# Optimization experiments

Hardware: AMD Instinct MI355X
Metric: run time of the kernel (lower is better)

## Reference

```python
import jax, jax.numpy as jnp
import numpy as np

B, T = 64, 2000
Q_DIM, MEM_DIM, ATT_DIM = 1024, 512, 128
N_FILTERS, KERNEL = 32, 31


def setup_inputs() -> dict:
    key = jax.random.key(0)
    ks = jax.random.split(key, 8)
    s = lambda fan_in: 1.0 / np.sqrt(fan_in)
    return {
        "attention_hidden_state": jax.random.normal(ks[0], (B, Q_DIM), jnp.float32),
        "memory": jax.random.normal(ks[1], (B, T, MEM_DIM), jnp.float32),
        "attention_weights_cat": jax.random.uniform(ks[2], (B, 2, T), jnp.float32),
        "W_query": jax.random.normal(ks[3], (Q_DIM, ATT_DIM), jnp.float32) * s(Q_DIM),
        "W_memory": jax.random.normal(ks[4], (MEM_DIM, ATT_DIM), jnp.float32) * s(MEM_DIM),
        "W_v": jax.random.normal(ks[5], (ATT_DIM, 1), jnp.float32) * s(ATT_DIM),
        "W_conv": jax.random.normal(ks[6], (KERNEL, 2, N_FILTERS), jnp.float32) * s(KERNEL * 2),  # WIO layout
        "W_loc": jax.random.normal(ks[7], (N_FILTERS, ATT_DIM), jnp.float32) * s(N_FILTERS),
    }


def reference(attention_hidden_state, memory, attention_weights_cat,
              W_query, W_memory, W_v, W_conv, W_loc):
    # processed query: [B, 1, D]
    pq = jnp.tanh(attention_hidden_state @ W_query)[:, None, :]
    # processed memory: [B, T, D]
    pm = jnp.tanh(jnp.einsum('btm,md->btd', memory, W_memory))
    # location features: Conv1D 'same', no bias, channels-last input [B, T, 2]
    awc = jnp.transpose(attention_weights_cat, (0, 2, 1))
    conv = jax.lax.conv_general_dilated(
        awc, W_conv, window_strides=(1,), padding='SAME',
        dimension_numbers=('NWC', 'WIO', 'NWC'))  # [B, T, F]
    ploc = jnp.tanh(conv @ W_loc)  # [B, T, D]
    # energies: [B, T]
    energies = jnp.squeeze(jnp.tanh(pq + ploc + pm) @ W_v, -1)
    attention_weights = jax.nn.softmax(energies, axis=1)  # [B, T]
    attention_context = jnp.einsum('bt,btm->bm', attention_weights, memory)
    return attention_context, attention_weights
```

## Files before the change

### kernel.cpp

```cpp
#include <hip/hip_runtime.h>
#include <hip/hip_bf16.h>

typedef __attribute__((ext_vector_type(8))) short s16x8;
typedef __attribute__((ext_vector_type(4))) float f32x4;

#define B_SZ 64
#define T_SZ 2000
#define QD 1024
#define MD 512
#define AD 128
#define NF 32
#define KW 31
#define NTILE 63
#define ASTRIDE 1056

__device__ __forceinline__ unsigned short f2bf(float f) {
    unsigned int u = __float_as_uint(f);
    unsigned int r = (u + 0x7FFFu + ((u >> 16) & 1u)) >> 16;
    return (unsigned short)r;
}
__device__ __forceinline__ unsigned int pack2bf_manual(float a, float b) {
    return (unsigned int)f2bf(a) | ((unsigned int)f2bf(b) << 16);
}
__device__ __forceinline__ unsigned int pack2bf(float a, float b) {
    union { __hip_bfloat162 h; unsigned int u; } cv;
    cv.h = __float22bfloat162_rn(float2{a, b});
    return cv.u;
}
__device__ __forceinline__ float fast_tanh(float x) {
    float ax = fabsf(x);
    float e = __expf(2.0f * ax);
    float r = 1.0f - 2.0f * __builtin_amdgcn_rcpf(e + 1.0f);
    return x < 0.0f ? -r : r;
}

__global__ __launch_bounds__(512) void prep_kernel(
    const float* __restrict__ ahs, const float* __restrict__ Wq,
    const float* __restrict__ Wm, const float* __restrict__ Wl,
    float* __restrict__ pq, unsigned short* __restrict__ WB,
    unsigned short* __restrict__ WL) {
    const int blk = blockIdx.x, tid = threadIdx.x;
    if (blk < 64) {
        __shared__ float q_sm[QD];
        __shared__ float part[3][AD];
        ((float2*)q_sm)[tid] = ((const float2*)(ahs + blk * QD))[tid];
        __syncthreads();
        const int d = tid & 127, kh = tid >> 7;
        const int k0 = kh * 256;
        float a0 = 0, a1 = 0, a2 = 0, a3 = 0;
        #pragma unroll 4
        for (int k = k0; k < k0 + 256; k += 4) {
            a0 += q_sm[k]     * Wq[(k)     * AD + d];
            a1 += q_sm[k + 1] * Wq[(k + 1) * AD + d];
            a2 += q_sm[k + 2] * Wq[(k + 2) * AD + d];
            a3 += q_sm[k + 3] * Wq[(k + 3) * AD + d];
        }
        float s = (a0 + a1) + (a2 + a3);
        if (kh) part[kh - 1][d] = s;
        __syncthreads();
        if (tid < AD)
            pq[blk * AD + tid] =
                fast_tanh((s + part[0][tid]) + (part[1][tid] + part[2][tid]));
    } else if (blk < 80) {
        int cidx = (blk - 64) * 512 + tid;
        int n = cidx >> 10, s = (cidx >> 6) & 15, l = cidx & 63;
        int col = n * 16 + (l & 15);
        int krow = s * 32 + (l >> 4) * 8;
        float v[8];
        #pragma unroll
        for (int j = 0; j < 8; ++j) v[j] = Wm[(krow + j) * AD + col];
        uint4 pk;
        pk.x = pack2bf(v[0], v[1]); pk.y = pack2bf(v[2], v[3]);
        pk.z = pack2bf(v[4], v[5]); pk.w = pack2bf(v[6], v[7]);
        *(uint4*)(WB + cidx * 8) = pk;
    } else {
        int cidx = tid;
        int n = cidx >> 6, l = cidx & 63;
        int col = n * 16 + (l & 15);
        int krow = (l >> 4) * 8;
        float v[8];
        #pragma unroll
        for (int j = 0; j < 8; ++j) v[j] = Wl[(krow + j) * AD + col];
        uint4 pk;
        pk.x = pack2bf_manual(v[0], v[1]); pk.y = pack2bf_manual(v[2], v[3]);
        pk.z = pack2bf_manual(v[4], v[5]); pk.w = pack2bf_manual(v[6], v[7]);
        *(uint4*)(WL + cidx * 8) = pk;
    }
}

__global__ __launch_bounds__(256) void energy_kernel(
    const float* __restrict__ memory, const float* __restrict__ awcat,
    const float* __restrict__ Wconv, const float* __restrict__ Wv,
    const float* __restrict__ pq, const unsigned short* __restrict__ WB,
    const unsigned short* __restrict__ WL, float* __restrict__ wts,
    float* __restrict__ ctile, float* __restrict__ mloc,
    float* __restrict__ Stile) {
    const int tile = blockIdx.x;
    const int b = blockIdx.y;
    const int t0 = tile * 32;
    const int tid = threadIdx.x;

    __shared__ __align__(16) unsigned short Atile[32 * (ASTRIDE / 2)];
    __shared__ float aw_sm[2][64];
    __shared__ __align__(16) unsigned short conv_sm[32 * 40];
    __shared__ float e_part[32][4];
    __shared__ float p_sm[32];

    if (tid < 128) {
        int c = tid >> 6, i = tid & 63;
        float v = 0.0f;
        int tv = t0 - 15 + i;
        if (i < 63 && tv >= 0 && tv < T_SZ) v = awcat[(b * 2 + c) * T_SZ + tv];
        aw_sm[c][i] = v;
    }

    {
        const float4* msrc = (const float4*)(memory + ((size_t)b * T_SZ + t0) * MD);
        #pragma unroll
        for (int it = 0; it < 8; ++it) {
            int cid = it * 256 + tid;
            int r = cid >> 6, cc = cid & 63;
            float4 v0 = {0, 0, 0, 0}, v1 = {0, 0, 0, 0};
            if (t0 + r < T_SZ) {
                v0 = msrc[r * 128 + cc * 2];
                v1 = msrc[r * 128 + cc * 2 + 1];
            }
            uint4 pk;
            pk.x = pack2bf(v0.x, v0.y); pk.y = pack2bf(v0.z, v0.w);
            pk.z = pack2bf(v1.x, v1.y); pk.w = pack2bf(v1.z, v1.w);
            int off = r * ASTRIDE + ((cc * 16) ^ ((r & 7) << 4));
            *(uint4*)((char*)Atile + off) = pk;
        }
    }
    __syncthreads();

    {
        int f = tid & 31, tq = tid >> 5;
        float acc[4] = {0, 0, 0, 0};
        for (int k = 0; k < KW; ++k) {
            #pragma unroll
            for (int c = 0; c < 2; ++c) {
                float wv = Wconv[(k * 2 + c) * NF + f];
                #pragma unroll
                for (int tt = 0; tt < 4; ++tt)
                    acc[tt] += wv * aw_sm[c][tq + tt * 8 + k];
            }
        }
        #pragma unroll
        for (int tt = 0; tt < 4; ++tt)
            conv_sm[(tq + tt * 8) * 40 + f] = f2bf(acc[tt]);
    }
    __syncthreads();

    const int w = tid >> 6, l = tid & 63;
    const int lr = l & 15, lg = l >> 4;
    const int d0 = (2 * w + 0) * 16 + lr;
    const int d1 = (2 * w + 1) * 16 + lr;
    const float pqv0 = pq[b * AD + d0], pqv1 = pq[b * AD + d1];
    const float wvv0 = Wv[d0], wvv1 = Wv[d1];

    f32x4 zero4 = {0, 0, 0, 0};
    f32x4 p00 = zero4, p01 = zero4, p10 = zero4, p11 = zero4;

    const s16x8* wbp = (const s16x8*)WB;
    const int swz = (lr & 7) << 4;
    const int rbase0 = lr * ASTRIDE;
    const int rbase1 = (16 + lr) * ASTRIDE;
    const int inb = lg * 16;

    #pragma unroll
    for (int s = 0; s < 16; ++s) {
        int j = (inb + s * 64) ^ swz;
        s16x8 a0 = *(const s16x8*)((const char*)Atile + rbase0 + j);
        s16x8 a1 = *(const s16x8*)((const char*)Atile + rbase1 + j);
        s16x8 b0 = wbp[((2 * w + 0) * 16 + s) * 64 + l];
        s16x8 b1 = wbp[((2 * w + 1) * 16 + s) * 64 + l];
        p00 = __builtin_amdgcn_mfma_f32_16x16x32_bf16(a0, b0, p00, 0, 0, 0);
        p01 = __builtin_amdgcn_mfma_f32_16x16x32_bf16(a0, b1, p01, 0, 0, 0);
        p10 = __builtin_amdgcn_mfma_f32_16x16x32_bf16(a1, b0, p10, 0, 0, 0);
        p11 = __builtin_amdgcn_mfma_f32_16x16x32_bf16(a1, b1, p11, 0, 0, 0);
    }

    s16x8 la0 = *(const s16x8*)((const char*)conv_sm + (lr * 80 + lg * 16));
    s16x8 la1 = *(const s16x8*)((const char*)conv_sm + ((16 + lr) * 80 + lg * 16));
    const s16x8* wlp = (const s16x8*)WL;
    s16x8 lb0 = wlp[(2 * w + 0) * 64 + l];
    s16x8 lb1 = wlp[(2 * w + 1) * 64 + l];
    f32x4 q00 = __builtin_amdgcn_mfma_f32_16x16x32_bf16(la0, lb0, zero4, 0, 0, 0);
    f32x4 q01 = __builtin_amdgcn_mfma_f32_16x16x32_bf16(la0, lb1, zero4, 0, 0, 0);
    f32x4 q10 = __builtin_amdgcn_mfma_f32_16x16x32_bf16(la1, lb0, zero4, 0, 0, 0);
    f32x4 q11 = __builtin_amdgcn_mfma_f32_16x16x32_bf16(la1, lb1, zero4, 0, 0, 0);

    float vr[8];
    #pragma unroll
    for (int r = 0; r < 4; ++r) {
        vr[r]     = fast_tanh(pqv0 + fast_tanh(q00[r]) + fast_tanh(p00[r])) * wvv0
                  + fast_tanh(pqv1 + fast_tanh(q01[r]) + fast_tanh(p01[r])) * wvv1;
        vr[4 + r] = fast_tanh(pqv0 + fast_tanh(q10[r]) + fast_tanh(p10[r])) * wvv0
                  + fast_tanh(pqv1 + fast_tanh(q11[r]) + fast_tanh(p11[r])) * wvv1;
    }
    #pragma unroll
    for (int j = 0; j < 8; ++j) {
        float v = vr[j];
        v += __shfl_xor(v, 1);
        v += __shfl_xor(v, 2);
        v += __shfl_xor(v, 4);
        v += __shfl_xor(v, 8);
        if (lr == 0) e_part[(j >> 2) * 16 + lg * 4 + (j & 3)][w] = v;
    }
    __syncthreads();

    if (tid < 32) {
        int t = t0 + tid;
        bool valid = t < T_SZ;
        float e = (e_part[tid][0] + e_part[tid][1]) + (e_part[tid][2] + e_part[tid][3]);
        float m = valid ? e : -3.4e38f;
        m = fmaxf(m, __shfl_xor(m, 1));
        m = fmaxf(m, __shfl_xor(m, 2));
        m = fmaxf(m, __shfl_xor(m, 4));
        m = fmaxf(m, __shfl_xor(m, 8));
        m = fmaxf(m, __shfl_xor(m, 16));
        float p = valid ? __expf(e - m) : 0.0f;
        p_sm[tid] = p;
        float S = p;
        S += __shfl_xor(S, 1);
        S += __shfl_xor(S, 2);
        S += __shfl_xor(S, 4);
        S += __shfl_xor(S, 8);
        S += __shfl_xor(S, 16);
        if (valid) wts[b * T_SZ + t] = p;
        if (tid == 0) { mloc[b * NTILE + tile] = m; Stile[b * NTILE + tile] = S; }
    }
    __syncthreads();

    {
        float c0 = 0.0f, c1 = 0.0f;
        const int boff = tid * 4;
        #pragma unroll
        for (int t = 0; t < 32; ++t) {
            float p = p_sm[t];
            unsigned int pk = *(const unsigned int*)(
                (const char*)Atile + t * ASTRIDE + (boff ^ ((t & 7) << 4)));
            c0 += p * __uint_as_float(pk << 16);
            c1 += p * __uint_as_float(pk & 0xffff0000u);
        }
        float2 o; o.x = c0; o.y = c1;
        ((float2*)ctile)[((b * NTILE + tile) << 8) + tid] = o;
    }
}

__global__ __launch_bounds__(256) void finalize_kernel(
    const float* __restrict__ mloc, const float* __restrict__ Stile,
    const float* __restrict__ ctile, float* __restrict__ wts,
    float* __restrict__ ctx) {
    const int b = blockIdx.x, h = blockIdx.y, tid = threadIdx.x;
    __shared__ float sc_sm[NTILE + 1];
    if (tid < 64) {
        float m = (tid < NTILE) ? mloc[b * NTILE + tid] : -3.4e38f;
        float s = (tid < NTILE) ? Stile[b * NTILE + tid] : 0.0f;
        float M = m;
        M = fmaxf(M, __shfl_xor(M, 1));  M = fmaxf(M, __shfl_xor(M, 2));
        M = fmaxf(M, __shfl_xor(M, 4));  M = fmaxf(M, __shfl_xor(M, 8));
        M = fmaxf(M, __shfl_xor(M, 16)); M = fmaxf(M, __shfl_xor(M, 32));
        float e = __expf(m - M);
        float z = e * s;
        z += __shfl_xor(z, 1);  z += __shfl_xor(z, 2);
        z += __shfl_xor(z, 4);  z += __shfl_xor(z, 8);
        z += __shfl_xor(z, 16); z += __shfl_xor(z, 32);
        if (tid < NTILE) sc_sm[tid] = e / z;
    }
    __syncthreads();

    if (h == 0) {
        #pragma unroll
        for (int i = 0; i < 8; ++i) {
            int idx = tid + i * 256;
            if (idx < T_SZ) wts[b * T_SZ + idx] *= sc_sm[idx >> 5];
        }
    }

    float a = 0.0f;
    const float* cb = ctile + ((size_t)b * NTILE << 9) + h * 256 + tid;
    #pragma unroll 7
    for (int tl = 0; tl < NTILE; ++tl) a += sc_sm[tl] * cb[(size_t)tl << 9];
    ctx[b * MD + h * 256 + tid] = a;
}

extern "C" void kernel_launch(void* const* d_in, const int* in_sizes, int n_in,
                              void* d_out, int out_size, void* d_ws, size_t ws_size,
                              hipStream_t stream) {
    const float* ahs    = (const float*)d_in[0];
    const float* memory = (const float*)d_in[1];
    const float* awcat  = (const float*)d_in[2];
    const float* Wq     = (const float*)d_in[3];
    const float* Wm     = (const float*)d_in[4];
    const float* Wv     = (const float*)d_in[5];
    const float* Wconv  = (const float*)d_in[6];
    const float* Wl     = (const float*)d_in[7];

    float* out = (float*)d_out;
    float* ctx = out;
    float* wts = out + B_SZ * MD;

    char* ws = (char*)d_ws;
    float* pq             = (float*)(ws);
    unsigned short* WB    = (unsigned short*)(ws + 32768);
    unsigned short* WL    = (unsigned short*)(ws + 163840);
    float* mloc           = (float*)(ws + 172032);
    float* Stile          = (float*)(ws + 188160);
    float* ctile          = (float*)(ws + 204800);

    prep_kernel<<<81, 512, 0, stream>>>(ahs, Wq, Wm, Wl, pq, WB, WL);
    energy_kernel<<<dim3(NTILE, B_SZ), 256, 0, stream>>>(
        memory, awcat, Wconv, Wv, pq, WB, WL, wts, ctile, mloc, Stile);
    finalize_kernel<<<dim3(B_SZ, 2), 256, 0, stream>>>(mloc, Stile, ctile, wts, ctx);
}
```

Baseline: 91.40 us.

## Halve energy tile to 16 timesteps and add unfused context fallback path

```diff
diff --git a/kernel.cpp b/kernel.cpp
--- a/kernel.cpp
+++ b/kernel.cpp
@@ -11,7 +11,8 @@
 #define AD 128
 #define NF 32
 #define KW 31
-#define NTILE 63
+#define TT 16
+#define NTILE 125
 #define ASTRIDE 1056
 
 __device__ __forceinline__ unsigned short f2bf(float f) {
@@ -88,43 +89,32 @@
     }
 }
 
-__global__ __launch_bounds__(256) void energy_kernel(
+__global__ __launch_bounds__(256, 6) void energy_kernel(
     const float* __restrict__ memory, const float* __restrict__ awcat,
     const float* __restrict__ Wconv, const float* __restrict__ Wv,
     const float* __restrict__ pq, const unsigned short* __restrict__ WB,
     const unsigned short* __restrict__ WL, float* __restrict__ wts,
     float* __restrict__ ctile, float* __restrict__ mloc,
-    float* __restrict__ Stile) {
+    float* __restrict__ Stile, int do_fuse) {
     const int tile = blockIdx.x;
     const int b = blockIdx.y;
-    const int t0 = tile * 32;
+    const int t0 = tile * TT;
     const int tid = threadIdx.x;
 
-    __shared__ __align__(16) unsigned short Atile[32 * (ASTRIDE / 2)];
+    __shared__ __align__(16) unsigned short Atile[TT * (ASTRIDE / 2)];
     __shared__ float aw_sm[2][64];
-    __shared__ __align__(16) unsigned short conv_sm[32 * 40];
-    __shared__ float e_part[32][4];
-    __shared__ float p_sm[32];
-
-    if (tid < 128) {
-        int c = tid >> 6, i = tid & 63;
-        float v = 0.0f;
-        int tv = t0 - 15 + i;
-        if (i < 63 && tv >= 0 && tv < T_SZ) v = awcat[(b * 2 + c) * T_SZ + tv];
-        aw_sm[c][i] = v;
-    }
+    __shared__ __align__(16) unsigned short conv_sm[TT * 40];
+    __shared__ float e_part[TT][4];
+    __shared__ float p_sm[TT];
 
     {
         const float4* msrc = (const float4*)(memory + ((size_t)b * T_SZ + t0) * MD);
         #pragma unroll
-        for (int it = 0; it < 8; ++it) {
+        for (int it = 0; it < 4; ++it) {
             int cid = it * 256 + tid;
             int r = cid >> 6, cc = cid & 63;
-            float4 v0 = {0, 0, 0, 0}, v1 = {0, 0, 0, 0};
-            if (t0 + r < T_SZ) {
-                v0 = msrc[r * 128 + cc * 2];
-                v1 = msrc[r * 128 + cc * 2 + 1];
-            }
+            float4 v0 = msrc[r * 128 + cc * 2];
+            float4 v1 = msrc[r * 128 + cc * 2 + 1];
             uint4 pk;
             pk.x = pack2bf(v0.x, v0.y); pk.y = pack2bf(v0.z, v0.w);
             pk.z = pack2bf(v1.x, v1.y); pk.w = pack2bf(v1.z, v1.w);
@@ -132,23 +122,29 @@
             *(uint4*)((char*)Atile + off) = pk;
         }
     }
+
+    if (tid < 128) {
+        int c = tid >> 6, i = tid & 63;
+        float v = 0.0f;
+        int tv = t0 - 15 + i;
+        if (i < 46 && tv >= 0 && tv < T_SZ) v = awcat[(b * 2 + c) * T_SZ + tv];
+        aw_sm[c][i] = v;
+    }
     __syncthreads();
 
     {
         int f = tid & 31, tq = tid >> 5;
-        float acc[4] = {0, 0, 0, 0};
+        float acc[2] = {0, 0};
         for (int k = 0; k < KW; ++k) {
             #pragma unroll
             for (int c = 0; c < 2; ++c) {
                 float wv = Wconv[(k * 2 + c) * NF + f];
-                #pragma unroll
-                for (int tt = 0; tt < 4; ++tt)
-                    acc[tt] += wv * aw_sm[c][tq + tt * 8 + k];
+                acc[0] += wv * aw_sm[c][tq + k];
+                acc[1] += wv * aw_sm[c][tq + 8 + k];
             }
         }
-        #pragma unroll
-        for (int tt = 0; tt < 4; ++tt)
-            conv_sm[(tq + tt * 8) * 40 + f] = f2bf(acc[tt]);
+        conv_sm[(tq)     * 40 + f] = f2bf(acc[0]);
+        conv_sm[(tq + 8) * 40 + f] = f2bf(acc[1]);
     }
     __syncthreads();
 
@@ -160,87 +156,70 @@
     const float wvv0 = Wv[d0], wvv1 = Wv[d1];
 
     f32x4 zero4 = {0, 0, 0, 0};
-    f32x4 p00 = zero4, p01 = zero4, p10 = zero4, p11 = zero4;
+    f32x4 p00 = zero4, p01 = zero4;
 
     const s16x8* wbp = (const s16x8*)WB;
     const int swz = (lr & 7) << 4;
-    const int rbase0 = lr * ASTRIDE;
-    const int rbase1 = (16 + lr) * ASTRIDE;
+    const int rbase = lr * ASTRIDE;
     const int inb = lg * 16;
+    const char* Ac = (const char*)Atile;
 
     #pragma unroll
     for (int s = 0; s < 16; ++s) {
         int j = (inb + s * 64) ^ swz;
-        s16x8 a0 = *(const s16x8*)((const char*)Atile + rbase0 + j);
-        s16x8 a1 = *(const s16x8*)((const char*)Atile + rbase1 + j);
+        s16x8 a0 = *(const s16x8*)(Ac + rbase + j);
         s16x8 b0 = wbp[((2 * w + 0) * 16 + s) * 64 + l];
         s16x8 b1 = wbp[((2 * w + 1) * 16 + s) * 64 + l];
         p00 = __builtin_amdgcn_mfma_f32_16x16x32_bf16(a0, b0, p00, 0, 0, 0);
         p01 = __builtin_amdgcn_mfma_f32_16x16x32_bf16(a0, b1, p01, 0, 0, 0);
-        p10 = __builtin_amdgcn_mfma_f32_16x16x32_bf16(a1, b0, p10, 0, 0, 0);
-        p11 = __builtin_amdgcn_mfma_f32_16x16x32_bf16(a1, b1, p11, 0, 0, 0);
     }
 
     s16x8 la0 = *(const s16x8*)((const char*)conv_sm + (lr * 80 + lg * 16));
-    s16x8 la1 = *(const s16x8*)((const char*)conv_sm + ((16 + lr) * 80 + lg * 16));
     const s16x8* wlp = (const s16x8*)WL;
     s16x8 lb0 = wlp[(2 * w + 0) * 64 + l];
     s16x8 lb1 = wlp[(2 * w + 1) * 64 + l];
     f32x4 q00 = __builtin_amdgcn_mfma_f32_16x16x32_bf16(la0, lb0, zero4, 0, 0, 0);
     f32x4 q01 = __builtin_amdgcn_mfma_f32_16x16x32_bf16(la0, lb1, zero4, 0, 0, 0);
-    f32x4 q10 = __builtin_amdgcn_mfma_f32_16x16x32_bf16(la1, lb0, zero4, 0, 0, 0);
-    f32x4 q11 = __builtin_amdgcn_mfma_f32_16x16x32_bf16(la1, lb1, zero4, 0, 0, 0);
-
-    float vr[8];
+
     #pragma unroll
     for (int r = 0; r < 4; ++r) {
-        vr[r]     = fast_tanh(pqv0 + fast_tanh(q00[r]) + fast_tanh(p00[r])) * wvv0
-                  + fast_tanh(pqv1 + fast_tanh(q01[r]) + fast_tanh(p01[r])) * wvv1;
-        vr[4 + r] = fast_tanh(pqv0 + fast_tanh(q10[r]) + fast_tanh(p10[r])) * wvv0
-                  + fast_tanh(pqv1 + fast_tanh(q11[r]) + fast_tanh(p11[r])) * wvv1;
-    }
-    #pragma unroll
-    for (int j = 0; j < 8; ++j) {
-        float v = vr[j];
+        float v = fast_tanh(pqv0 + fast_tanh(q00[r]) + fast_tanh(p00[r])) * wvv0
+                + fast_tanh(pqv1 + fast_tanh(q01[r]) + fast_tanh(p01[r])) * wvv1;
         v += __shfl_xor(v, 1);
         v += __shfl_xor(v, 2);
         v += __shfl_xor(v, 4);
         v += __shfl_xor(v, 8);
-        if (lr == 0) e_part[(j >> 2) * 16 + lg * 4 + (j & 3)][w] = v;
-    }
-    __syncthreads();
-
-    if (tid < 32) {
-        int t = t0 + tid;
-        bool valid = t < T_SZ;
+        if (lr == 0) e_part[lg * 4 + r][w] = v;
+    }
+    __syncthreads();
+
+    if (tid < TT) {
         float e = (e_part[tid][0] + e_part[tid][1]) + (e_part[tid][2] + e_part[tid][3]);
-        float m = valid ? e : -3.4e38f;
+        float m = e;
         m = fmaxf(m, __shfl_xor(m, 1));
         m = fmaxf(m, __shfl_xor(m, 2));
         m = fmaxf(m, __shfl_xor(m, 4));
         m = fmaxf(m, __shfl_xor(m, 8));
-        m = fmaxf(m, __shfl_xor(m, 16));
-        float p = valid ? __expf(e - m) : 0.0f;
+        float p = __expf(e - m);
         p_sm[tid] = p;
         float S = p;
         S += __shfl_xor(S, 1);
         S += __shfl_xor(S, 2);
         S += __shfl_xor(S, 4);
         S += __shfl_xor(S, 8);
-        S += __shfl_xor(S, 16);
-        if (valid) wts[b * T_SZ + t] = p;
+        wts[b * T_SZ + t0 + tid] = p;
         if (tid == 0) { mloc[b * NTILE + tile] = m; Stile[b * NTILE + tile] = S; }
     }
     __syncthreads();
 
-    {
+    if (do_fuse) {
         float c0 = 0.0f, c1 = 0.0f;
         const int boff = tid * 4;
         #pragma unroll
-        for (int t = 0; t < 32; ++t) {
+        for (int t = 0; t < TT; ++t) {
             float p = p_sm[t];
             unsigned int pk = *(const unsigned int*)(
-                (const char*)Atile + t * ASTRIDE + (boff ^ ((t & 7) << 4)));
+                Ac + t * ASTRIDE + (boff ^ ((t & 7) << 4)));
             c0 += p * __uint_as_float(pk << 16);
             c1 += p * __uint_as_float(pk & 0xffff0000u);
         }
@@ -252,22 +231,27 @@
 __global__ __launch_bounds__(256) void finalize_kernel(
     const float* __restrict__ mloc, const float* __restrict__ Stile,
     const float* __restrict__ ctile, float* __restrict__ wts,
-    float* __restrict__ ctx) {
+    float* __restrict__ ctx, int do_fuse) {
     const int b = blockIdx.x, h = blockIdx.y, tid = threadIdx.x;
-    __shared__ float sc_sm[NTILE + 1];
+    __shared__ float sc_sm[128];
     if (tid < 64) {
-        float m = (tid < NTILE) ? mloc[b * NTILE + tid] : -3.4e38f;
-        float s = (tid < NTILE) ? Stile[b * NTILE + tid] : 0.0f;
-        float M = m;
+        float ma = mloc[b * NTILE + tid];
+        float sa = Stile[b * NTILE + tid];
+        bool hasb = (tid + 64) < NTILE;
+        float mb = hasb ? mloc[b * NTILE + tid + 64] : -3.4e38f;
+        float sb = hasb ? Stile[b * NTILE + tid + 64] : 0.0f;
+        float M = fmaxf(ma, mb);
         M = fmaxf(M, __shfl_xor(M, 1));  M = fmaxf(M, __shfl_xor(M, 2));
         M = fmaxf(M, __shfl_xor(M, 4));  M = fmaxf(M, __shfl_xor(M, 8));
         M = fmaxf(M, __shfl_xor(M, 16)); M = fmaxf(M, __shfl_xor(M, 32));
-        float e = __expf(m - M);
-        float z = e * s;
+        float ea = __expf(ma - M), eb = hasb ? __expf(mb - M) : 0.0f;
+        float z = ea * sa + eb * sb;
         z += __shfl_xor(z, 1);  z += __shfl_xor(z, 2);
         z += __shfl_xor(z, 4);  z += __shfl_xor(z, 8);
         z += __shfl_xor(z, 16); z += __shfl_xor(z, 32);
-        if (tid < NTILE) sc_sm[tid] = e / z;
+        float inv = 1.0f / z;
+        sc_sm[tid] = ea * inv;
+        sc_sm[tid + 64] = eb * inv;
     }
     __syncthreads();
 
@@ -275,15 +259,47 @@
         #pragma unroll
         for (int i = 0; i < 8; ++i) {
             int idx = tid + i * 256;
-            if (idx < T_SZ) wts[b * T_SZ + idx] *= sc_sm[idx >> 5];
-        }
-    }
-
-    float a = 0.0f;
-    const float* cb = ctile + ((size_t)b * NTILE << 9) + h * 256 + tid;
-    #pragma unroll 7
-    for (int tl = 0; tl < NTILE; ++tl) a += sc_sm[tl] * cb[(size_t)tl << 9];
-    ctx[b * MD + h * 256 + tid] = a;
+            if (idx < T_SZ) wts[b * T_SZ + idx] *= sc_sm[idx >> 4];
+        }
+    }
+
+    if (do_fuse) {
+        float a = 0.0f;
+        const float* cb = ctile + ((size_t)b * NTILE << 9) + h * 256 + tid;
+        #pragma unroll 5
+        for (int tl = 0; tl < NTILE; ++tl) a += sc_sm[tl] * cb[(size_t)tl << 9];
+        ctx[b * MD + h * 256 + tid] = a;
+    }
+}
+
+__global__ __launch_bounds__(256) void ctx_partial_kernel(
+    const float* __restrict__ memory, const float* __restrict__ wts,
+    float* __restrict__ part) {
+    const int ci = blockIdx.x, b = blockIdx.y, tid = threadIdx.x;
+    const float2* m2 = (const float2*)memory;
+    float2 acc = {0.0f, 0.0f};
+    const int t0 = ci * 100, t1 = t0 + 100;
+    #pragma unroll 4
+    for (int t = t0; t < t1; ++t) {
+        float wgt = wts[b * T_SZ + t];
+        float2 v = m2[((size_t)(b * T_SZ + t)) * 256 + tid];
+        acc.x += wgt * v.x;
+        acc.y += wgt * v.y;
+    }
+    ((float2*)part)[(b * 20 + ci) * 256 + tid] = acc;
+}
+__global__ __launch_bounds__(256) void ctx_reduce_kernel(
+    const float* __restrict__ part, float* __restrict__ ctx) {
+    const int b = blockIdx.x, tid = threadIdx.x;
+    const float2* p2 = (const float2*)part;
+    float2 acc = {0.0f, 0.0f};
+    #pragma unroll
+    for (int ci = 0; ci < 20; ++ci) {
+        float2 v = p2[(b * 20 + ci) * 256 + tid];
+        acc.x += v.x;
+        acc.y += v.y;
+    }
+    ((float2*)ctx)[b * 256 + tid] = acc;
 }
 
 extern "C" void kernel_launch(void* const* d_in, const int* in_sizes, int n_in,
@@ -307,11 +323,20 @@
     unsigned short* WB    = (unsigned short*)(ws + 32768);
     unsigned short* WL    = (unsigned short*)(ws + 163840);
     float* mloc           = (float*)(ws + 172032);
-    float* Stile          = (float*)(ws + 188160);
-    float* ctile          = (float*)(ws + 204800);
+    float* Stile          = (float*)(ws + 204800);
+    float* ctile          = (float*)(ws + 237568);
+    float* part           = (float*)(ws + 237568);
+
+    const size_t need_fused = 237568 + (size_t)B_SZ * NTILE * MD * 4;
+    const int do_fuse = (ws_size >= need_fused) ? 1 : 0;
 
     prep_kernel<<<81, 512, 0, stream>>>(ahs, Wq, Wm, Wl, pq, WB, WL);
     energy_kernel<<<dim3(NTILE, B_SZ), 256, 0, stream>>>(
-        memory, awcat, Wconv, Wv, pq, WB, WL, wts, ctile, mloc, Stile);
-    finalize_kernel<<<dim3(B_SZ, 2), 256, 0, stream>>>(mloc, Stile, ctile, wts, ctx);
-}
+        memory, awcat, Wconv, Wv, pq, WB, WL, wts, ctile, mloc, Stile, do_fuse);
+    finalize_kernel<<<dim3(B_SZ, 2), 256, 0, stream>>>(
+        mloc, Stile, ctile, wts, ctx, do_fuse);
+    if (!do_fuse) {
+        ctx_partial_kernel<<<dim3(20, B_SZ), 256, 0, stream>>>(memory, wts, part);
+        ctx_reduce_kernel<<<B_SZ, 256, 0, stream>>>(part, ctx);
+    }
+}
```

New measurement: 103.4 us. 1.13x slower.

## Feed MFMA operands directly from global memory instead of staging in LDS

Applied to the files above, without the earlier changes.

```diff
diff --git a/kernel.cpp b/kernel.cpp
--- a/kernel.cpp
+++ b/kernel.cpp
@@ -12,7 +12,6 @@
 #define NF 32
 #define KW 31
 #define NTILE 63
-#define ASTRIDE 1056
 
 __device__ __forceinline__ unsigned short f2bf(float f) {
     unsigned int u = __float_as_uint(f);
@@ -26,6 +25,12 @@
     union { __hip_bfloat162 h; unsigned int u; } cv;
     cv.h = __float22bfloat162_rn(float2{a, b});
     return cv.u;
+}
+__device__ __forceinline__ s16x8 pack8(float4 x0, float4 x1) {
+    union { s16x8 v; uint4 u; } r;
+    r.u.x = pack2bf(x0.x, x0.y); r.u.y = pack2bf(x0.z, x0.w);
+    r.u.z = pack2bf(x1.x, x1.y); r.u.w = pack2bf(x1.z, x1.w);
+    return r.v;
 }
 __device__ __forceinline__ float fast_tanh(float x) {
     float ax = fabsf(x);
@@ -88,7 +93,7 @@
     }
 }
 
-__global__ __launch_bounds__(256) void energy_kernel(
+__global__ __launch_bounds__(256, 4) void energy_kernel(
     const float* __restrict__ memory, const float* __restrict__ awcat,
     const float* __restrict__ Wconv, const float* __restrict__ Wv,
     const float* __restrict__ pq, const unsigned short* __restrict__ WB,
@@ -99,8 +104,8 @@
     const int b = blockIdx.y;
     const int t0 = tile * 32;
     const int tid = threadIdx.x;
-
-    __shared__ __align__(16) unsigned short Atile[32 * (ASTRIDE / 2)];
+    const bool full = (t0 + 32 <= T_SZ);
+
     __shared__ float aw_sm[2][64];
     __shared__ __align__(16) unsigned short conv_sm[32 * 40];
     __shared__ float e_part[32][4];
@@ -112,25 +117,6 @@
         int tv = t0 - 15 + i;
         if (i < 63 && tv >= 0 && tv < T_SZ) v = awcat[(b * 2 + c) * T_SZ + tv];
         aw_sm[c][i] = v;
-    }
-
-    {
-        const float4* msrc = (const float4*)(memory + ((size_t)b * T_SZ + t0) * MD);
-        #pragma unroll
-        for (int it = 0; it < 8; ++it) {
-            int cid = it * 256 + tid;
-            int r = cid >> 6, cc = cid & 63;
-            float4 v0 = {0, 0, 0, 0}, v1 = {0, 0, 0, 0};
-            if (t0 + r < T_SZ) {
-                v0 = msrc[r * 128 + cc * 2];
-                v1 = msrc[r * 128 + cc * 2 + 1];
-            }
-            uint4 pk;
-            pk.x = pack2bf(v0.x, v0.y); pk.y = pack2bf(v0.z, v0.w);
-            pk.z = pack2bf(v1.x, v1.y); pk.w = pack2bf(v1.z, v1.w);
-            int off = r * ASTRIDE + ((cc * 16) ^ ((r & 7) << 4));
-            *(uint4*)((char*)Atile + off) = pk;
-        }
     }
     __syncthreads();
 
@@ -163,22 +149,33 @@
     f32x4 p00 = zero4, p01 = zero4, p10 = zero4, p11 = zero4;
 
     const s16x8* wbp = (const s16x8*)WB;
-    const int swz = (lr & 7) << 4;
-    const int rbase0 = lr * ASTRIDE;
-    const int rbase1 = (16 + lr) * ASTRIDE;
-    const int inb = lg * 16;
-
-    #pragma unroll
-    for (int s = 0; s < 16; ++s) {
-        int j = (inb + s * 64) ^ swz;
-        s16x8 a0 = *(const s16x8*)((const char*)Atile + rbase0 + j);
-        s16x8 a1 = *(const s16x8*)((const char*)Atile + rbase1 + j);
-        s16x8 b0 = wbp[((2 * w + 0) * 16 + s) * 64 + l];
-        s16x8 b1 = wbp[((2 * w + 1) * 16 + s) * 64 + l];
-        p00 = __builtin_amdgcn_mfma_f32_16x16x32_bf16(a0, b0, p00, 0, 0, 0);
-        p01 = __builtin_amdgcn_mfma_f32_16x16x32_bf16(a0, b1, p01, 0, 0, 0);
-        p10 = __builtin_amdgcn_mfma_f32_16x16x32_bf16(a1, b0, p10, 0, 0, 0);
-        p11 = __builtin_amdgcn_mfma_f32_16x16x32_bf16(a1, b1, p11, 0, 0, 0);
+    const float4* m0 = (const float4*)(memory + ((size_t)b * T_SZ + t0 + lr) * MD) + lg * 2;
+
+    if (full) {
+        const float4* m1 = m0 + 16 * (MD / 4);
+        #pragma unroll 4
+        for (int s = 0; s < 16; ++s) {
+            float4 x0 = m0[s * 8], x1 = m0[s * 8 + 1];
+            float4 y0 = m1[s * 8], y1 = m1[s * 8 + 1];
+            s16x8 b0 = wbp[((2 * w + 0) * 16 + s) * 64 + l];
+            s16x8 b1 = wbp[((2 * w + 1) * 16 + s) * 64 + l];
+            s16x8 a0 = pack8(x0, x1);
+            s16x8 a1 = pack8(y0, y1);
+            p00 = __builtin_amdgcn_mfma_f32_16x16x32_bf16(a0, b0, p00, 0, 0, 0);
+            p01 = __builtin_amdgcn_mfma_f32_16x16x32_bf16(a0, b1, p01, 0, 0, 0);
+            p10 = __builtin_amdgcn_mfma_f32_16x16x32_bf16(a1, b0, p10, 0, 0, 0);
+            p11 = __builtin_amdgcn_mfma_f32_16x16x32_bf16(a1, b1, p11, 0, 0, 0);
+        }
+    } else {
+        #pragma unroll 4
+        for (int s = 0; s < 16; ++s) {
+            float4 x0 = m0[s * 8], x1 = m0[s * 8 + 1];
+            s16x8 b0 = wbp[((2 * w + 0) * 16 + s) * 64 + l];
+            s16x8 b1 = wbp[((2 * w + 1) * 16 + s) * 64 + l];
+            s16x8 a0 = pack8(x0, x1);
+            p00 = __builtin_amdgcn_mfma_f32_16x16x32_bf16(a0, b0, p00, 0, 0, 0);
+            p01 = __builtin_amdgcn_mfma_f32_16x16x32_bf16(a0, b1, p01, 0, 0, 0);
+        }
     }
 
     s16x8 la0 = *(const s16x8*)((const char*)conv_sm + (lr * 80 + lg * 16));
@@ -201,12 +198,12 @@
     }
     #pragma unroll
     for (int j = 0; j < 8; ++j) {
-        float v = vr[j];
-        v += __shfl_xor(v, 1);
-        v += __shfl_xor(v, 2);
-        v += __shfl_xor(v, 4);
-        v += __shfl_xor(v, 8);
-        if (lr == 0) e_part[(j >> 2) * 16 + lg * 4 + (j & 3)][w] = v;
+        float vv = vr[j];
+        vv += __shfl_xor(vv, 1);
+        vv += __shfl_xor(vv, 2);
+        vv += __shfl_xor(vv, 4);
+        vv += __shfl_xor(vv, 8);
+        if (lr == 0) e_part[(j >> 2) * 16 + lg * 4 + (j & 3)][w] = vv;
     }
     __syncthreads();
 
@@ -234,15 +231,24 @@
     __syncthreads();
 
     {
+        const float2* mr = (const float2*)(memory + ((size_t)b * T_SZ + t0) * MD);
         float c0 = 0.0f, c1 = 0.0f;
-        const int boff = tid * 4;
-        #pragma unroll
-        for (int t = 0; t < 32; ++t) {
-            float p = p_sm[t];
-            unsigned int pk = *(const unsigned int*)(
-                (const char*)Atile + t * ASTRIDE + (boff ^ ((t & 7) << 4)));
-            c0 += p * __uint_as_float(pk << 16);
-            c1 += p * __uint_as_float(pk & 0xffff0000u);
+        if (full) {
+            #pragma unroll 8
+            for (int t = 0; t < 32; ++t) {
+                float p = p_sm[t];
+                float2 v = mr[t * 256 + tid];
+                c0 += p * v.x;
+                c1 += p * v.y;
+            }
+        } else {
+            #pragma unroll 8
+            for (int t = 0; t < 16; ++t) {
+                float p = p_sm[t];
+                float2 v = mr[t * 256 + tid];
+                c0 += p * v.x;
+                c1 += p * v.y;
+            }
         }
         float2 o; o.x = c0; o.y = c1;
         ((float2*)ctile)[((b * NTILE + tile) << 8) + tid] = o;
```

After: 180.3 us. +97.2%, slower.

## Double energy kernel block to 512 threads, one 16-wide D slice per wave

Applied to the files above, without the earlier changes.

```diff
diff --git a/kernel.cpp b/kernel.cpp
--- a/kernel.cpp
+++ b/kernel.cpp
@@ -88,7 +88,7 @@
     }
 }
 
-__global__ __launch_bounds__(256) void energy_kernel(
+__global__ __launch_bounds__(512, 8) void energy_kernel(
     const float* __restrict__ memory, const float* __restrict__ awcat,
     const float* __restrict__ Wconv, const float* __restrict__ Wv,
     const float* __restrict__ pq, const unsigned short* __restrict__ WB,
@@ -103,22 +103,15 @@
     __shared__ __align__(16) unsigned short Atile[32 * (ASTRIDE / 2)];
     __shared__ float aw_sm[2][64];
     __shared__ __align__(16) unsigned short conv_sm[32 * 40];
-    __shared__ float e_part[32][4];
+    __shared__ float e_part[32][8];
+    __shared__ float e_sm[32];
     __shared__ float p_sm[32];
-
-    if (tid < 128) {
-        int c = tid >> 6, i = tid & 63;
-        float v = 0.0f;
-        int tv = t0 - 15 + i;
-        if (i < 63 && tv >= 0 && tv < T_SZ) v = awcat[(b * 2 + c) * T_SZ + tv];
-        aw_sm[c][i] = v;
-    }
 
     {
         const float4* msrc = (const float4*)(memory + ((size_t)b * T_SZ + t0) * MD);
         #pragma unroll
-        for (int it = 0; it < 8; ++it) {
-            int cid = it * 256 + tid;
+        for (int it = 0; it < 4; ++it) {
+            int cid = it * 512 + tid;
             int r = cid >> 6, cc = cid & 63;
             float4 v0 = {0, 0, 0, 0}, v1 = {0, 0, 0, 0};
             if (t0 + r < T_SZ) {
@@ -132,89 +125,97 @@
             *(uint4*)((char*)Atile + off) = pk;
         }
     }
+
+    if (tid < 128) {
+        int c = tid >> 6, i = tid & 63;
+        float v = 0.0f;
+        int tv = t0 - 15 + i;
+        if (i < 63 && tv >= 0 && tv < T_SZ) v = awcat[(b * 2 + c) * T_SZ + tv];
+        aw_sm[c][i] = v;
+    }
     __syncthreads();
 
     {
         int f = tid & 31, tq = tid >> 5;
-        float acc[4] = {0, 0, 0, 0};
+        float acc0 = 0, acc1 = 0;
         for (int k = 0; k < KW; ++k) {
             #pragma unroll
             for (int c = 0; c < 2; ++c) {
                 float wv = Wconv[(k * 2 + c) * NF + f];
-                #pragma unroll
-                for (int tt = 0; tt < 4; ++tt)
-                    acc[tt] += wv * aw_sm[c][tq + tt * 8 + k];
+                acc0 += wv * aw_sm[c][tq + k];
+                acc1 += wv * aw_sm[c][tq + 16 + k];
             }
         }
-        #pragma unroll
-        for (int tt = 0; tt < 4; ++tt)
-            conv_sm[(tq + tt * 8) * 40 + f] = f2bf(acc[tt]);
+        conv_sm[(tq)      * 40 + f] = f2bf(acc0);
+        conv_sm[(tq + 16) * 40 + f] = f2bf(acc1);
     }
     __syncthreads();
 
     const int w = tid >> 6, l = tid & 63;
     const int lr = l & 15, lg = l >> 4;
-    const int d0 = (2 * w + 0) * 16 + lr;
-    const int d1 = (2 * w + 1) * 16 + lr;
-    const float pqv0 = pq[b * AD + d0], pqv1 = pq[b * AD + d1];
-    const float wvv0 = Wv[d0], wvv1 = Wv[d1];
+    const int d = w * 16 + lr;
+    const float pqv = pq[b * AD + d];
+    const float wvv = Wv[d];
 
     f32x4 zero4 = {0, 0, 0, 0};
-    f32x4 p00 = zero4, p01 = zero4, p10 = zero4, p11 = zero4;
+    f32x4 p00 = zero4, p10 = zero4;
 
     const s16x8* wbp = (const s16x8*)WB;
     const int swz = (lr & 7) << 4;
     const int rbase0 = lr * ASTRIDE;
     const int rbase1 = (16 + lr) * ASTRIDE;
     const int inb = lg * 16;
+    const char* Ac = (const char*)Atile;
 
     #pragma unroll
     for (int s = 0; s < 16; ++s) {
         int j = (inb + s * 64) ^ swz;
-        s16x8 a0 = *(const s16x8*)((const char*)Atile + rbase0 + j);
-        s16x8 a1 = *(const s16x8*)((const char*)Atile + rbase1 + j);
-        s16x8 b0 = wbp[((2 * w + 0) * 16 + s) * 64 + l];
-        s16x8 b1 = wbp[((2 * w + 1) * 16 + s) * 64 + l];
-        p00 = __builtin_amdgcn_mfma_f32_16x16x32_bf16(a0, b0, p00, 0, 0, 0);
-        p01 = __builtin_amdgcn_mfma_f32_16x16x32_bf16(a0, b1, p01, 0, 0, 0);
-        p10 = __builtin_amdgcn_mfma_f32_16x16x32_bf16(a1, b0, p10, 0, 0, 0);
-        p11 = __builtin_amdgcn_mfma_f32_16x16x32_bf16(a1, b1, p11, 0, 0, 0);
+        s16x8 a0 = *(const s16x8*)(Ac + rbase0 + j);
+        s16x8 a1 = *(const s16x8*)(Ac + rbase1 + j);
+        s16x8 bf = wbp[(w * 16 + s) * 64 + l];
+        p00 = __builtin_amdgcn_mfma_f32_16x16x32_bf16(a0, bf, p00, 0, 0, 0);
+        p10 = __builtin_amdgcn_mfma_f32_16x16x32_bf16(a1, bf, p10, 0, 0, 0);
     }
 
     s16x8 la0 = *(const s16x8*)((const char*)conv_sm + (lr * 80 + lg * 16));
     s16x8 la1 = *(const s16x8*)((const char*)conv_sm + ((16 + lr) * 80 + lg * 16));
     const s16x8* wlp = (const s16x8*)WL;
-    s16x8 lb0 = wlp[(2 * w + 0) * 64 + l];
-    s16x8 lb1 = wlp[(2 * w + 1) * 64 + l];
-    f32x4 q00 = __builtin_amdgcn_mfma_f32_16x16x32_bf16(la0, lb0, zero4, 0, 0, 0);
-    f32x4 q01 = __builtin_amdgcn_mfma_f32_16x16x32_bf16(la0, lb1, zero4, 0, 0, 0);
-    f32x4 q10 = __builtin_amdgcn_mfma_f32_16x16x32_bf16(la1, lb0, zero4, 0, 0, 0);
-    f32x4 q11 = __builtin_amdgcn_mfma_f32_16x16x32_bf16(la1, lb1, zero4, 0, 0, 0);
-
-    float vr[8];
+    s16x8 lb = wlp[w * 64 + l];
+    f32x4 q00 = __builtin_amdgcn_mfma_f32_16x16x32_bf16(la0, lb, zero4, 0, 0, 0);
+    f32x4 q10 = __builtin_amdgcn_mfma_f32_16x16x32_bf16(la1, lb, zero4, 0, 0, 0);
+
     #pragma unroll
     for (int r = 0; r < 4; ++r) {
-        vr[r]     = fast_tanh(pqv0 + fast_tanh(q00[r]) + fast_tanh(p00[r])) * wvv0
-                  + fast_tanh(pqv1 + fast_tanh(q01[r]) + fast_tanh(p01[r])) * wvv1;
-        vr[4 + r] = fast_tanh(pqv0 + fast_tanh(q10[r]) + fast_tanh(p10[r])) * wvv0
-                  + fast_tanh(pqv1 + fast_tanh(q11[r]) + fast_tanh(p11[r])) * wvv1;
-    }
-    #pragma unroll
-    for (int j = 0; j < 8; ++j) {
-        float v = vr[j];
+        float v0 = fast_tanh(pqv + fast_tanh(q00[r]) + fast_tanh(p00[r])) * wvv;
+        v0 += __shfl_xor(v0, 1);
+        v0 += __shfl_xor(v0, 2);
+        v0 += __shfl_xor(v0, 4);
+        v0 += __shfl_xor(v0, 8);
+        if (lr == 0) e_part[lg * 4 + r][w] = v0;
+        float v1 = fast_tanh(pqv + fast_tanh(q10[r]) + fast_tanh(p10[r])) * wvv;
+        v1 += __shfl_xor(v1, 1);
+        v1 += __shfl_xor(v1, 2);
+        v1 += __shfl_xor(v1, 4);
+        v1 += __shfl_xor(v1, 8);
+        if (lr == 0) e_part[16 + lg * 4 + r][w] = v1;
+    }
+    __syncthreads();
+
+    if (tid < 256) {
+        int t = tid >> 3, g = tid & 7;
+        float v = e_part[t][g];
         v += __shfl_xor(v, 1);
         v += __shfl_xor(v, 2);
         v += __shfl_xor(v, 4);
-        v += __shfl_xor(v, 8);
-        if (lr == 0) e_part[(j >> 2) * 16 + lg * 4 + (j & 3)][w] = v;
+        if (g == 0) e_sm[t] = (t0 + t < T_SZ) ? v : -3.4e38f;
     }
     __syncthreads();
 
     if (tid < 32) {
         int t = t0 + tid;
         bool valid = t < T_SZ;
-        float e = (e_part[tid][0] + e_part[tid][1]) + (e_part[tid][2] + e_part[tid][3]);
-        float m = valid ? e : -3.4e38f;
+        float e = e_sm[tid];
+        float m = e;
         m = fmaxf(m, __shfl_xor(m, 1));
         m = fmaxf(m, __shfl_xor(m, 2));
         m = fmaxf(m, __shfl_xor(m, 4));
@@ -234,18 +235,16 @@
     __syncthreads();
 
     {
-        float c0 = 0.0f, c1 = 0.0f;
-        const int boff = tid * 4;
+        float c = 0.0f;
+        const int boff = 2 * tid;
         #pragma unroll
         for (int t = 0; t < 32; ++t) {
             float p = p_sm[t];
-            unsigned int pk = *(const unsigned int*)(
-                (const char*)Atile + t * ASTRIDE + (boff ^ ((t & 7) << 4)));
-            c0 += p * __uint_as_float(pk << 16);
-            c1 += p * __uint_as_float(pk & 0xffff0000u);
-        }
-        float2 o; o.x = c0; o.y = c1;
-        ((float2*)ctile)[((b * NTILE + tile) << 8) + tid] = o;
+            unsigned short us = *(const unsigned short*)(
+                Ac + t * ASTRIDE + (boff ^ ((t & 7) << 4)));
+            c += p * __uint_as_float(((unsigned int)us) << 16);
+        }
+        ctile[(((size_t)b * NTILE + tile) << 9) + tid] = c;
     }
 }
 
@@ -311,7 +310,7 @@
     float* ctile          = (float*)(ws + 204800);
 
     prep_kernel<<<81, 512, 0, stream>>>(ahs, Wq, Wm, Wl, pq, WB, WL);
-    energy_kernel<<<dim3(NTILE, B_SZ), 256, 0, stream>>>(
+    energy_kernel<<<dim3(NTILE, B_SZ), 512, 0, stream>>>(
         memory, awcat, Wconv, Wv, pq, WB, WL, wts, ctile, mloc, Stile);
     finalize_kernel<<<dim3(B_SZ, 2), 256, 0, stream>>>(mloc, Stile, ctile, wts, ctx);
 }
```

After: 104.9 us. +14.7%, slower.
